# Performance work log

Hardware: AMD Instinct MI355X
Metric: run time of the kernel (lower is better)

Reference implementation:

```python
import jax, jax.numpy as jnp
import numpy as np

B = 262144
D = 128          # state_dim
L = 8            # levels
STOP_THRESHOLD = 0.6
LN_EPS = 1e-5


def setup_inputs() -> dict:
    key = jax.random.key(0)
    ks = jax.random.split(key, 4)
    signal = jax.random.normal(ks[0], (B, D), dtype=jnp.float32)
    previous = jax.random.normal(ks[1], (B, D), dtype=jnp.float32)
    # nn.Linear default init: U(-1/sqrt(fan_in), 1/sqrt(fan_in)), fan_in = 2D
    bound = 1.0 / np.sqrt(2 * D)
    Wp = jax.random.uniform(ks[2], (L, 2 * D, D), jnp.float32, -bound, bound)  # projection weight (in, out)
    bp = jax.random.uniform(ks[3], (L, D), jnp.float32, -bound, bound)
    # _reset_parameters: gate weight zeros, gate bias -1.2; stop head all zeros
    Wg = jnp.zeros((L, 2 * D, D), jnp.float32)
    bg = jnp.full((L, D), -1.2, jnp.float32)
    Ws = jnp.zeros((L, 2 * D, 1), jnp.float32)
    bs = jnp.zeros((L, 1), jnp.float32)
    gamma = jnp.ones((L, D), jnp.float32)   # LayerNorm weight
    beta = jnp.zeros((L, D), jnp.float32)   # LayerNorm bias
    return {"signal": signal, "previous": previous, "Wp": Wp, "bp": bp,
            "Wg": Wg, "bg": bg, "Ws": Ws, "bs": bs, "gamma": gamma, "beta": beta}


def _layernorm(x, gamma, beta):
    mu = jnp.mean(x, axis=-1, keepdims=True)
    var = jnp.mean(jnp.square(x - mu), axis=-1, keepdims=True)
    return (x - mu) * jax.lax.rsqrt(var + LN_EPS) * gamma + beta


def reference(signal, previous, Wp, bp, Wg, bg, Ws, bs, gamma, beta):
    levels = jnp.arange(1, L + 1, dtype=signal.dtype)

    def step(carry, xs):
        current, acc, active, depth, smass = carry
        Wp_l, bp_l, Wg_l, bg_l, Ws_l, bs_l, g_l, b_l, lvl = xs
        joined = jnp.concatenate([current, previous], axis=-1)           # [B, 2D]
        gate = jax.nn.sigmoid(joined @ Wg_l + bg_l)                      # [B, D]
        candidate = jnp.tanh(joined @ Wp_l + bp_l)                       # [B, D]
        updated = _layernorm(current + gate * (candidate - current), g_l, b_l)
        joined2 = jnp.concatenate([updated, previous], axis=-1)
        adequacy = jax.nn.sigmoid(joined2 @ Ws_l + bs_l)                 # [B, 1]
        stop_prob = jax.nn.sigmoid((adequacy - STOP_THRESHOLD) * 10.0)
        stop_mass = active * stop_prob
        acc = acc + stop_mass * updated
        active = active * (1.0 - stop_prob)
        depth = depth + stop_mass * lvl
        smass = smass + stop_mass
        stats = (jnp.mean(gate, axis=-1),                                # gate mean  [B]
                 jnp.linalg.norm(updated - current, axis=-1),            # delta norm [B]
                 adequacy[:, 0])                                         # adequacy   [B]
        return (updated, acc, active, depth, smass), stats

    init = (signal,
            jnp.zeros_like(signal),
            jnp.ones((signal.shape[0], 1), signal.dtype),
            jnp.zeros((signal.shape[0], 1), signal.dtype),
            jnp.zeros((signal.shape[0], 1), signal.dtype))
    (current, acc, active, depth, smass), (gates, deltas, adeqs) = jax.lax.scan(
        step, init, (Wp, bp, Wg, bg, Ws, bs, gamma, beta, levels))

    accumulated = acc + active * current
    stop_depth = depth + active * float(L)
    gate_mean = jnp.mean(gates, axis=0)       # mean over levels -> [B]
    delta_mean = jnp.mean(deltas, axis=0)
    adequacy_mean = jnp.mean(adeqs, axis=0)
    return (accumulated, gate_mean, delta_mean,
            stop_depth[:, 0], smass[:, 0], adequacy_mean)
```

## Files before the change

kernel.cpp:

```cpp
#include <hip/hip_runtime.h>
#include <math.h>

#define NB 262144
#define ND 128
#define NL 8

typedef __bf16 bf16x8 __attribute__((ext_vector_type(8)));
typedef float  f32x4  __attribute__((ext_vector_type(4)));

union BFP { unsigned int u; __bf16 h[2]; unsigned short s[2]; };
union F4  { float4 f; float a[4]; };

__device__ __forceinline__ float sigm(float x){ return 1.0f/(1.0f + __expf(-x)); }
__device__ __forceinline__ float tanhfast(float x){
  float t = __expf(-2.0f*fabsf(x));
  return copysignf((1.0f - t)/(1.0f + t), x);
}
__device__ __forceinline__ float redrow(float v){
  v += __shfl_xor(v, 16);
  v += __shfl_xor(v, 32);
  return v;
}
__device__ __forceinline__ unsigned int pk2(float a, float b){
  BFP x; x.h[0]=(__bf16)a; x.h[1]=(__bf16)b; return x.u;
}
__device__ __forceinline__ float ubf(unsigned int u, int hi){
  BFP x; x.u = u; return (float)x.h[hi];
}
__device__ __forceinline__ void gload16(const void* g, void* s){
  __builtin_amdgcn_global_load_lds((const __attribute__((address_space(1))) unsigned int*)g,
                                   (__attribute__((address_space(3))) unsigned int*)s,
                                   16, 0, 0);
}

__global__ void repack_w(const float* __restrict__ Wp, const float* __restrict__ Wg,
                         uint4* __restrict__ dst){
  int t = blockIdx.x*256 + threadIdx.x;
  int lane = t & 63;
  int frag = t >> 6;
  int cf = frag & 7, kf = (frag >> 3) & 7, mat = (frag >> 6) & 1, l = frag >> 7;
  const float* W = mat ? Wp : Wg;
  int k = kf*32 + (lane >> 4)*8;
  int n = cf*16 + (lane & 15);
  const float* src = W + (l*256 + k)*ND + n;
  bf16x8 v;
#pragma unroll
  for (int j=0;j<8;++j) v[j] = (__bf16)src[j*ND];
  dst[((l*2 + mat)*64 + kf*8 + cf)*64 + lane] = __builtin_bit_cast(uint4, v);
}

__global__ void prevdot_k(const float* __restrict__ previous, const float* __restrict__ Ws,
                          const float* __restrict__ bs, float* __restrict__ pdot){
  int t = blockIdx.x*256 + threadIdx.x;
  int row = t >> 4, g = t & 15;
  const float* p = previous + (size_t)row*ND + g*8;
  float4 a = *(const float4*)p;
  float4 b = *(const float4*)(p+4);
#pragma unroll
  for (int l=0;l<NL;++l){
    const float* w = Ws + l*256 + 128 + g*8;
    float s = a.x*w[0] + a.y*w[1] + a.z*w[2] + a.w*w[3]
            + b.x*w[4] + b.y*w[5] + b.z*w[6] + b.w*w[7];
    s += __shfl_xor(s,1); s += __shfl_xor(s,2); s += __shfl_xor(s,4); s += __shfl_xor(s,8);
    if (g==0) pdot[row*NL + l] = s + bs[l];
  }
}

__global__ __launch_bounds__(512)
void fused_k(const float* __restrict__ signal, const float* __restrict__ previous,
             const float* __restrict__ bp, const float* __restrict__ bg,
             const float* __restrict__ Ws, const float* __restrict__ gamma,
             const float* __restrict__ beta,
             const uint4* __restrict__ wpk, const float* __restrict__ pdot,
             float* __restrict__ out)
{
  __shared__ unsigned short tile[128*256];
  __shared__ uint4 wbuf[2][512];

  const int tid  = threadIdx.x;
  const int w    = tid >> 6;
  const int lane = tid & 63;
  const int llo  = lane & 15;
  const int lhi  = lane >> 4;
  const int rbase = w * 16;
  const int row0  = blockIdx.x * 128;
  const int swz   = (llo & 7) << 4;

  auto gstage = [&](int s, int b){
    gload16((const char*)wpk + (size_t)s*8192 + tid*16, (char*)&wbuf[b][0] + tid*16);
  };
  gstage(0, 0);

  unsigned int gstash[16];
  float accv[8][4];
  f32x4 pacc[8];
  float active, depth, smass, gsum, dsum, asum;

  {
    int rl = rbase + llo;
    int rowg = row0 + rl;
#pragma unroll
    for (int cf=0; cf<8; ++cf){
      F4 v; v.f = *(const float4*)&signal[(size_t)rowg*ND + 16*cf + 4*lhi];
      unsigned p0 = pk2(v.a[0], v.a[1]);
      unsigned p1 = pk2(v.a[2], v.a[3]);
      char* dst = (char*)tile + rl*512 + ((32*cf + 8*lhi) ^ swz);
      *(unsigned long long*)dst = (unsigned long long)p0 | ((unsigned long long)p1 << 32);
      pacc[cf] = (f32x4){0.f,0.f,0.f,0.f};
#pragma unroll
      for (int j=0;j<4;++j) accv[cf][j] = 0.f;
    }
#pragma unroll
    for (int kfp=0; kfp<4; ++kfp){
      const float* p = previous + (size_t)rowg*ND + kfp*32 + lhi*8;
      F4 a; a.f = *(const float4*)p;
      F4 b; b.f = *(const float4*)(p+4);
      uint4 pv;
      pv.x = pk2(a.a[0], a.a[1]);
      pv.y = pk2(a.a[2], a.a[3]);
      pv.z = pk2(b.a[0], b.a[1]);
      pv.w = pk2(b.a[2], b.a[3]);
      char* dst = (char*)tile + rl*512 + ((256 + 64*kfp + 16*lhi) ^ swz);
      *(uint4*)dst = pv;
    }
    active=1.f; depth=0.f; smass=0.f; gsum=0.f; dsum=0.f; asum=0.f;
  }

  auto compute = [&](int s){
    int kf  = s & 7;
    int buf = s & 1;
    int off = (64*kf + 16*lhi) ^ swz;
    bf16x8 xf = __builtin_bit_cast(bf16x8,
        *(const uint4*)((const char*)tile + (rbase + llo)*512 + off));
    const uint4* wb = &wbuf[buf][lane];
#pragma unroll
    for (int cf=0; cf<8; ++cf){
      bf16x8 wf = __builtin_bit_cast(bf16x8, wb[cf*64]);
      pacc[cf] = __builtin_amdgcn_mfma_f32_16x16x32_bf16(wf, xf, pacc[cf], 0,0,0);
    }
  };

  auto gate_epi = [&](int lev){
    float gp = 0.f;
#pragma unroll
    for (int cf=0; cf<8; ++cf){
      F4 bgv; bgv.f = *(const float4*)&bg[lev*ND + 16*cf + 4*lhi];
      float g0 = sigm(pacc[cf][0] + bgv.a[0]);
      float g1 = sigm(pacc[cf][1] + bgv.a[1]);
      float g2 = sigm(pacc[cf][2] + bgv.a[2]);
      float g3 = sigm(pacc[cf][3] + bgv.a[3]);
      gp += g0 + g1 + g2 + g3;
      gstash[2*cf]   = pk2(g0, g1);
      gstash[2*cf+1] = pk2(g2, g3);
      pacc[cf] = (f32x4){0.f,0.f,0.f,0.f};
    }
    gsum += redrow(gp) * (1.0f/ND);
  };

  auto cand_epi = [&](int lev, bool wr){
    int rl = rbase + llo;
    int rowg = row0 + rl;
    char* cbase = (char*)tile + rl*512;
    float s1 = 0.f, s2 = 0.f;
#pragma unroll
    for (int cf=0; cf<8; ++cf){
      F4 bpv; bpv.f = *(const float4*)&bp[lev*ND + 16*cf + 4*lhi];
      unsigned long long cw = *(const unsigned long long*)(cbase + ((32*cf + 8*lhi) ^ swz));
      unsigned c0 = (unsigned)cw, c1 = (unsigned)(cw >> 32);
#pragma unroll
      for (int j=0;j<4;++j){
        float cand = tanhfast(pacc[cf][j] + bpv.a[j]);
        float cc = ubf(j<2 ? c0 : c1, j&1);
        float gt = ubf(gstash[2*cf + (j>>1)], j&1);
        float x = cc + gt*(cand - cc);
        pacc[cf][j] = x;
        s1 += x; s2 += x*x;
      }
    }
    s1 = redrow(s1); s2 = redrow(s2);
    float mu  = s1*(1.0f/ND);
    float inv = rsqrtf(s2*(1.0f/ND) - mu*mu + 1e-5f);
    float dp = 0.f, ap = 0.f;
#pragma unroll
    for (int cf=0; cf<8; ++cf){
      F4 gm; gm.f = *(const float4*)&gamma[lev*ND + 16*cf + 4*lhi];
      F4 bt; bt.f = *(const float4*)&beta [lev*ND + 16*cf + 4*lhi];
      F4 wv; wv.f = *(const float4*)&Ws   [lev*2*ND + 16*cf + 4*lhi];
      unsigned long long cw = *(const unsigned long long*)(cbase + ((32*cf + 8*lhi) ^ swz));
      unsigned c0 = (unsigned)cw, c1 = (unsigned)(cw >> 32);
#pragma unroll
      for (int j=0;j<4;++j){
        float un = (pacc[cf][j] - mu)*inv*gm.a[j] + bt.a[j];
        float cc = ubf(j<2 ? c0 : c1, j&1);
        float df = un - cc;
        dp += df*df;
        ap += un*wv.a[j];
        pacc[cf][j] = un;
      }
    }
    dp = redrow(dp); ap = redrow(ap);
    float adq = sigm(ap + pdot[(size_t)rowg*NL + lev]);
    float sp  = sigm((adq - 0.6f)*10.0f);
    float sm  = active*sp;
    asum += adq;
    dsum += sqrtf(dp);
    depth += sm * (float)(lev+1);
    smass += sm;
    active *= (1.0f - sp);
#pragma unroll
    for (int cf=0; cf<8; ++cf){
#pragma unroll
      for (int j=0;j<4;++j) accv[cf][j] += sm * pacc[cf][j];
      if (wr){
        unsigned p0 = pk2(pacc[cf][0], pacc[cf][1]);
        unsigned p1 = pk2(pacc[cf][2], pacc[cf][3]);
        char* dst = cbase + ((32*cf + 8*lhi) ^ swz);
        *(unsigned long long*)dst = (unsigned long long)p0 | ((unsigned long long)p1 << 32);
        pacc[cf] = (f32x4){0.f,0.f,0.f,0.f};
      }
    }
    if (wr){
      asm volatile("s_waitcnt lgkmcnt(0)" ::: "memory");
      __builtin_amdgcn_sched_barrier(0);
    }
  };

#pragma unroll 1
  for (int l=0; l<NL; ++l){
#pragma unroll 1
    for (int q=0; q<16; ++q){
      int s = l*16 + q;
      __syncthreads();
      if (s+1 < 128) gstage(s+1, (s+1)&1);
      if (q == 8) gate_epi(l);
      if (q == 0 && l > 0) cand_epi(l-1, true);
      compute(s);
    }
  }
  cand_epi(NL-1, false);

  {
    int rowg = row0 + rbase + llo;
#pragma unroll
    for (int cf=0; cf<8; ++cf){
      F4 o;
#pragma unroll
      for (int j=0;j<4;++j)
        o.a[j] = accv[cf][j] + active*pacc[cf][j];
      *(float4*)&out[(size_t)rowg*ND + 16*cf + 4*lhi] = o.f;
    }
    if (lhi == 0){
      const size_t BD = (size_t)NB*ND;
      out[BD + rowg]                = gsum*(1.0f/NL);
      out[BD + NB + rowg]           = dsum*(1.0f/NL);
      out[BD + 2*(size_t)NB + rowg] = depth + active*(float)NL;
      out[BD + 3*(size_t)NB + rowg] = smass;
      out[BD + 4*(size_t)NB + rowg] = asum*(1.0f/NL);
    }
  }
}

extern "C" void kernel_launch(void* const* d_in, const int* in_sizes, int n_in,
                              void* d_out, int out_size, void* d_ws, size_t ws_size,
                              hipStream_t stream){
  const float* signal   = (const float*)d_in[0];
  const float* previous = (const float*)d_in[1];
  const float* Wp    = (const float*)d_in[2];
  const float* bp    = (const float*)d_in[3];
  const float* Wg    = (const float*)d_in[4];
  const float* bg    = (const float*)d_in[5];
  const float* Ws    = (const float*)d_in[6];
  const float* bs    = (const float*)d_in[7];
  const float* gamma = (const float*)d_in[8];
  const float* beta  = (const float*)d_in[9];

  uint4* wpk  = (uint4*)d_ws;
  float* pdot = (float*)((char*)d_ws + (size_t)NL*2*65536);

  repack_w<<<256, 256, 0, stream>>>(Wp, Wg, wpk);
  prevdot_k<<<NB/16, 256, 0, stream>>>(previous, Ws, bs, pdot);
  fused_k<<<NB/128, 512, 0, stream>>>(signal, previous, bp, bg, Ws, gamma, beta,
                                      wpk, pdot, (float*)d_out);
}
```

Measured before the change: 1.045 ms.

## Triple-buffer weight staging, keep previous in registers, cache params in LDS

Weight-tile staging moves from a double buffer to a triple buffer with prefetch distance two. Each step now waits with explicit vmcnt counts and a raw s_barrier instead of __syncthreads, so global loads stay in flight across steps. The loop-invariant 'previous' bf16 fragments are kept in registers rather than the LDS tile, which halves the tile size. Per-level bias, gamma, beta, Ws and a transposed pdot slab are preloaded into shared memory to take global loads out of the epilogues. This raises LDS use and register pressure, and relies on the hand-written waitcnt sequencing being correct.

```diff
diff --git a/kernel.cpp b/kernel.cpp
--- a/kernel.cpp
+++ b/kernel.cpp
@@ -4,6 +4,7 @@
 #define NB 262144
 #define ND 128
 #define NL 8
+#define TOT (NL*16)
 
 typedef __bf16 bf16x8 __attribute__((ext_vector_type(8)));
 typedef float  f32x4  __attribute__((ext_vector_type(4)));
@@ -62,7 +63,7 @@
     float s = a.x*w[0] + a.y*w[1] + a.z*w[2] + a.w*w[3]
             + b.x*w[4] + b.y*w[5] + b.z*w[6] + b.w*w[7];
     s += __shfl_xor(s,1); s += __shfl_xor(s,2); s += __shfl_xor(s,4); s += __shfl_xor(s,8);
-    if (g==0) pdot[row*NL + l] = s + bs[l];
+    if (g==0) pdot[(size_t)l*NB + row] = s + bs[l];
   }
 }
 
@@ -74,8 +75,10 @@
              const uint4* __restrict__ wpk, const float* __restrict__ pdot,
              float* __restrict__ out)
 {
-  __shared__ unsigned short tile[128*256];
-  __shared__ uint4 wbuf[2][512];
+  __shared__ unsigned short tile[128*128];
+  __shared__ uint4 wbuf[3][512];
+  __shared__ float cst[5*1024];
+  __shared__ float pdl[1024];
 
   const int tid  = threadIdx.x;
   const int w    = tid >> 6;
@@ -89,11 +92,21 @@
   auto gstage = [&](int s, int b){
     gload16((const char*)wpk + (size_t)s*8192 + tid*16, (char*)&wbuf[b][0] + tid*16);
   };
-  gstage(0, 0);
+
+#pragma unroll
+  for (int i = tid; i < 1024; i += 512){
+    cst[i]        = bg[i];
+    cst[1024 + i] = bp[i];
+    cst[2048 + i] = gamma[i];
+    cst[3072 + i] = beta[i];
+    cst[4096 + i] = Ws[(i >> 7)*256 + (i & 127)];
+    pdl[i]        = pdot[(size_t)(i >> 7)*NB + row0 + (i & 127)];
+  }
 
   unsigned int gstash[16];
   float accv[8][4];
   f32x4 pacc[8];
+  bf16x8 prevB[4];
   float active, depth, smass, gsum, dsum, asum;
 
   {
@@ -104,7 +117,7 @@
       F4 v; v.f = *(const float4*)&signal[(size_t)rowg*ND + 16*cf + 4*lhi];
       unsigned p0 = pk2(v.a[0], v.a[1]);
       unsigned p1 = pk2(v.a[2], v.a[3]);
-      char* dst = (char*)tile + rl*512 + ((32*cf + 8*lhi) ^ swz);
+      char* dst = (char*)tile + rl*256 + ((32*cf + 8*lhi) ^ swz);
       *(unsigned long long*)dst = (unsigned long long)p0 | ((unsigned long long)p1 << 32);
       pacc[cf] = (f32x4){0.f,0.f,0.f,0.f};
 #pragma unroll
@@ -120,18 +133,24 @@
       pv.y = pk2(a.a[2], a.a[3]);
       pv.z = pk2(b.a[0], b.a[1]);
       pv.w = pk2(b.a[2], b.a[3]);
-      char* dst = (char*)tile + rl*512 + ((256 + 64*kfp + 16*lhi) ^ swz);
-      *(uint4*)dst = pv;
+      prevB[kfp] = __builtin_bit_cast(bf16x8, pv);
     }
     active=1.f; depth=0.f; smass=0.f; gsum=0.f; dsum=0.f; asum=0.f;
   }
-
-  auto compute = [&](int s){
-    int kf  = s & 7;
-    int buf = s & 1;
-    int off = (64*kf + 16*lhi) ^ swz;
-    bf16x8 xf = __builtin_bit_cast(bf16x8,
-        *(const uint4*)((const char*)tile + (rbase + llo)*512 + off));
+  __syncthreads();
+  gstage(0, 0);
+  gstage(1, 1);
+
+  auto compute = [&](int s, int buf){
+    int kf = s & 7;
+    bf16x8 xf;
+    if (kf < 4){
+      int off = (64*kf + 16*lhi) ^ swz;
+      xf = __builtin_bit_cast(bf16x8,
+          *(const uint4*)((const char*)tile + (rbase + llo)*256 + off));
+    } else {
+      xf = prevB[kf-4];
+    }
     const uint4* wb = &wbuf[buf][lane];
 #pragma unroll
     for (int cf=0; cf<8; ++cf){
@@ -144,7 +163,7 @@
     float gp = 0.f;
 #pragma unroll
     for (int cf=0; cf<8; ++cf){
-      F4 bgv; bgv.f = *(const float4*)&bg[lev*ND + 16*cf + 4*lhi];
+      F4 bgv; bgv.f = *(const float4*)&cst[lev*128 + 16*cf + 4*lhi];
       float g0 = sigm(pacc[cf][0] + bgv.a[0]);
       float g1 = sigm(pacc[cf][1] + bgv.a[1]);
       float g2 = sigm(pacc[cf][2] + bgv.a[2]);
@@ -159,12 +178,11 @@
 
   auto cand_epi = [&](int lev, bool wr){
     int rl = rbase + llo;
-    int rowg = row0 + rl;
-    char* cbase = (char*)tile + rl*512;
+    char* cbase = (char*)tile + rl*256;
     float s1 = 0.f, s2 = 0.f;
 #pragma unroll
     for (int cf=0; cf<8; ++cf){
-      F4 bpv; bpv.f = *(const float4*)&bp[lev*ND + 16*cf + 4*lhi];
+      F4 bpv; bpv.f = *(const float4*)&cst[1024 + lev*128 + 16*cf + 4*lhi];
       unsigned long long cw = *(const unsigned long long*)(cbase + ((32*cf + 8*lhi) ^ swz));
       unsigned c0 = (unsigned)cw, c1 = (unsigned)(cw >> 32);
 #pragma unroll
@@ -183,9 +201,9 @@
     float dp = 0.f, ap = 0.f;
 #pragma unroll
     for (int cf=0; cf<8; ++cf){
-      F4 gm; gm.f = *(const float4*)&gamma[lev*ND + 16*cf + 4*lhi];
-      F4 bt; bt.f = *(const float4*)&beta [lev*ND + 16*cf + 4*lhi];
-      F4 wv; wv.f = *(const float4*)&Ws   [lev*2*ND + 16*cf + 4*lhi];
+      F4 gm; gm.f = *(const float4*)&cst[2048 + lev*128 + 16*cf + 4*lhi];
+      F4 bt; bt.f = *(const float4*)&cst[3072 + lev*128 + 16*cf + 4*lhi];
+      F4 wv; wv.f = *(const float4*)&cst[4096 + lev*128 + 16*cf + 4*lhi];
       unsigned long long cw = *(const unsigned long long*)(cbase + ((32*cf + 8*lhi) ^ swz));
       unsigned c0 = (unsigned)cw, c1 = (unsigned)(cw >> 32);
 #pragma unroll
@@ -199,7 +217,7 @@
       }
     }
     dp = redrow(dp); ap = redrow(ap);
-    float adq = sigm(ap + pdot[(size_t)rowg*NL + lev]);
+    float adq = sigm(ap + pdl[lev*128 + rl]);
     float sp  = sigm((adq - 0.6f)*10.0f);
     float sm  = active*sp;
     asum += adq;
@@ -225,17 +243,22 @@
     }
   };
 
+  int bufc = 0;
 #pragma unroll 1
-  for (int l=0; l<NL; ++l){
-#pragma unroll 1
-    for (int q=0; q<16; ++q){
-      int s = l*16 + q;
-      __syncthreads();
-      if (s+1 < 128) gstage(s+1, (s+1)&1);
-      if (q == 8) gate_epi(l);
-      if (q == 0 && l > 0) cand_epi(l-1, true);
-      compute(s);
-    }
+  for (int s=0; s<TOT; ++s){
+    if (s < TOT-1) asm volatile("s_waitcnt vmcnt(1)" ::: "memory");
+    else           asm volatile("s_waitcnt vmcnt(0)" ::: "memory");
+    __builtin_amdgcn_s_barrier();
+    __builtin_amdgcn_sched_barrier(0);
+    if (s+2 < TOT){
+      int b2 = bufc + 2; if (b2 >= 3) b2 -= 3;
+      gstage(s+2, b2);
+    }
+    int q = s & 15, l = s >> 4;
+    if (q == 8) gate_epi(l);
+    else if (q == 0 && l > 0) cand_epi(l-1, true);
+    compute(s, bufc);
+    bufc = (bufc == 2) ? 0 : bufc + 1;
   }
   cand_epi(NL-1, false);
 
```

Result: slower. 1.205 ms (+15.3%).
